# Kernel tuning notes

Hardware: AMD Instinct MI355X
Metric: run time of the kernel (lower is better)

The kernel has to match this reference:

```python
import jax, jax.numpy as jnp
import numpy as np

N, C, H, W = 4, 64, 64, 64
EPS = 1e-5


def setup_inputs() -> dict:
    key = jax.random.key(0)
    ks = jax.random.split(key, 8)
    f = lambda k, s: jax.random.normal(k, s, dtype=jnp.float32)
    return {
        "low_feats": f(ks[0], (N, C, H, W)),
        "heat0": f(ks[1], (N, C, H, W)),
        "heat1": f(ks[2], (N, C, H, W)),
        # f_query: 1x1 conv + BN(gamma,beta) + ReLU
        "Wq": f(ks[3], (C, C)) * 0.05, "bq": jnp.zeros((C,), jnp.float32),
        "gq": jnp.ones((C,), jnp.float32), "betaq": jnp.zeros((C,), jnp.float32),
        # f_key: 1x1 conv + BN + ReLU
        "Wk": f(ks[4], (C, C)) * 0.05, "bk": jnp.zeros((C,), jnp.float32),
        "gk": jnp.ones((C,), jnp.float32), "betak": jnp.zeros((C,), jnp.float32),
        # f_value: plain 1x1 conv
        "Wv": f(ks[5], (C, C)) * 0.05, "bv": jnp.zeros((C,), jnp.float32),
    }


def _conv1x1(x, Wc, bc):
    # [N,C,H,W] -> [N,O,H,W]
    return jnp.einsum("oc,nchw->nohw", Wc, x) + bc[None, :, None, None]


def _conv_bn_relu(x, Wc, bc, g, beta):
    y = _conv1x1(x, Wc, bc)
    mu = y.mean(axis=(0, 2, 3), keepdims=True)      # batch-stat BN (train mode)
    var = y.var(axis=(0, 2, 3), keepdims=True)
    y = (y - mu) * jax.lax.rsqrt(var + EPS)
    y = y * g[None, :, None, None] + beta[None, :, None, None]
    return jax.nn.relu(y)


def reference(low_feats, heat0, heat1, Wq, bq, gq, betaq, Wk, bk, gk, betak, Wv, bv):
    n, c, h, w = low_feats.shape
    hw = h * w
    query = _conv_bn_relu(low_feats, Wq, bq, gq, betaq).reshape(n, c, hw).transpose(0, 2, 1)  # [N,HW,C]
    keym = _conv_bn_relu(low_feats, Wk, bk, gk, betak).reshape(n, c, hw)                      # [N,C,HW]
    value = _conv1x1(low_feats, Wv, bv).reshape(n, c, hw).transpose(0, 2, 1)                  # [N,HW,C]
    sim = jax.nn.softmax(jnp.einsum("nqc,nck->nqk", query, keym), axis=-1)                    # [N,HW,HW]
    # dual gated value paths share the softmax map: sim@vI + sim@vC == sim@(vI+vC)
    gate = (heat0 + heat1).reshape(n, c, hw).transpose(0, 2, 1)                               # [N,HW,C]
    gated_v = gate * value
    ctx = jnp.einsum("nqk,nkc->nqc", sim, gated_v)                                            # [N,HW,C]
    return ctx.transpose(0, 2, 1).reshape(n, c, h, w)
```

## Files before the change

### kernel.cpp

```cpp
#include <hip/hip_runtime.h>

#define NB 4
#define CC 64
#define HW 4096
#define NT (NB*HW)
#define EPSV 1e-5f
#define LOG2E 1.4426950408889634f

typedef _Float16 f16;
typedef _Float16 half4 __attribute__((ext_vector_type(4)));
typedef _Float16 half8 __attribute__((ext_vector_type(8)));
typedef float   float4v __attribute__((ext_vector_type(4)));

#define NELEM ((size_t)NB*HW*CC)
#define NSLOT 128

#define PART_OFF 512
#define TEN_OFF  264192

__global__ __launch_bounds__(256)
void conv2_kernel(const float* __restrict__ x,
                  const float* __restrict__ h0, const float* __restrict__ h1,
                  const float* __restrict__ Wq, const float* __restrict__ bq,
                  const float* __restrict__ Wk, const float* __restrict__ bk,
                  const float* __restrict__ Wv, const float* __restrict__ bv,
                  float* __restrict__ ws,
                  f16* __restrict__ q, f16* __restrict__ k, f16* __restrict__ gv)
{
    __shared__ float Wl[3][16*CC];
    __shared__ float xs[CC][128];
    const int t    = threadIdx.x;
    const int n    = blockIdx.y;
    const int z    = blockIdx.z;
    const int px0  = blockIdx.x * 128;
    const int lane = t & 63;
    const int grp  = t >> 6;
    const int ocl  = grp * 4;
    const int oc0  = z*16 + ocl;

    ((float4*)Wl[0])[t] = ((const float4*)(Wq + (size_t)z*16*CC))[t];
    ((float4*)Wl[1])[t] = ((const float4*)(Wk + (size_t)z*16*CC))[t];
    ((float4*)Wl[2])[t] = ((const float4*)(Wv + (size_t)z*16*CC))[t];
    for (int i = t; i < CC*32; i += 256) {
        int ic = i >> 5, c4 = i & 31;
        ((float4*)&xs[ic][0])[c4] =
            ((const float4*)(x + ((size_t)n*CC + ic)*HW + px0))[c4];
    }
    __syncthreads();

    float aq[4][2], ak[4][2], av[4][2];
    #pragma unroll
    for (int j = 0; j < 4; ++j) {
        aq[j][0] = aq[j][1] = bq[oc0+j];
        ak[j][0] = ak[j][1] = bk[oc0+j];
        av[j][0] = av[j][1] = bv[oc0+j];
    }

    for (int ic = 0; ic < CC; ic += 4) {
        float2 xv0 = *(float2*)&xs[ic  ][lane*2];
        float2 xv1 = *(float2*)&xs[ic+1][lane*2];
        float2 xv2 = *(float2*)&xs[ic+2][lane*2];
        float2 xv3 = *(float2*)&xs[ic+3][lane*2];
        #pragma unroll
        for (int j = 0; j < 4; ++j) {
            const int row = (ocl+j)*CC + ic;
            float4 wq = *(const float4*)&Wl[0][row];
            float4 wk = *(const float4*)&Wl[1][row];
            float4 wv = *(const float4*)&Wl[2][row];
            aq[j][0] = fmaf(wq.x,xv0.x, fmaf(wq.y,xv1.x, fmaf(wq.z,xv2.x, fmaf(wq.w,xv3.x, aq[j][0]))));
            aq[j][1] = fmaf(wq.x,xv0.y, fmaf(wq.y,xv1.y, fmaf(wq.z,xv2.y, fmaf(wq.w,xv3.y, aq[j][1]))));
            ak[j][0] = fmaf(wk.x,xv0.x, fmaf(wk.y,xv1.x, fmaf(wk.z,xv2.x, fmaf(wk.w,xv3.x, ak[j][0]))));
            ak[j][1] = fmaf(wk.x,xv0.y, fmaf(wk.y,xv1.y, fmaf(wk.z,xv2.y, fmaf(wk.w,xv3.y, ak[j][1]))));
            av[j][0] = fmaf(wv.x,xv0.x, fmaf(wv.y,xv1.x, fmaf(wv.z,xv2.x, fmaf(wv.w,xv3.x, av[j][0]))));
            av[j][1] = fmaf(wv.x,xv0.y, fmaf(wv.y,xv1.y, fmaf(wv.z,xv2.y, fmaf(wv.w,xv3.y, av[j][1]))));
        }
    }

    const int px = px0 + lane*2;
    const size_t base = ((size_t)n*HW + px)*CC + oc0;
    half4 vq0, vq1, vk0, vk1;
    #pragma unroll
    for (int j = 0; j < 4; ++j) {
        vq0[j] = (f16)aq[j][0]; vq1[j] = (f16)aq[j][1];
        vk0[j] = (f16)ak[j][0]; vk1[j] = (f16)ak[j][1];
    }
    *(half4*)&q[base]      = vq0;  *(half4*)&q[base + CC] = vq1;
    *(half4*)&k[base]      = vk0;  *(half4*)&k[base + CC] = vk1;

    #pragma unroll
    for (int j = 0; j < 4; ++j) {
        size_t gi = ((size_t)n*CC + oc0 + j)*HW + px;
        f16 g0 = (f16)((h0[gi]   + h1[gi]  ) * av[j][0]);
        f16 g1 = (f16)((h0[gi+1] + h1[gi+1]) * av[j][1]);
        gv[gi]   = g0;
        gv[gi+1] = g1;
    }

    float* slot = ws + PART_OFF + (size_t)(n*(HW/128) + blockIdx.x)*256;
    #pragma unroll
    for (int j = 0; j < 4; ++j) {
        float v0 = aq[j][0] + aq[j][1];
        float v1 = aq[j][0]*aq[j][0] + aq[j][1]*aq[j][1];
        float v2 = ak[j][0] + ak[j][1];
        float v3 = ak[j][0]*ak[j][0] + ak[j][1]*ak[j][1];
        #pragma unroll
        for (int off = 32; off > 0; off >>= 1) {
            v0 += __shfl_down(v0, off);
            v1 += __shfl_down(v1, off);
            v2 += __shfl_down(v2, off);
            v3 += __shfl_down(v3, off);
        }
        if (lane == 0) {
            slot[      oc0 + j] = v0;
            slot[ 64 + oc0 + j] = v1;
            slot[128 + oc0 + j] = v2;
            slot[192 + oc0 + j] = v3;
        }
    }
}

__global__ __launch_bounds__(256)
void apply_kernel(f16* __restrict__ q, f16* __restrict__ k,
                  const float* __restrict__ ws,
                  const float* __restrict__ gq, const float* __restrict__ betaq,
                  const float* __restrict__ gk, const float* __restrict__ betak)
{
    __shared__ float tot[128];
    __shared__ float sc[CC], sh[CC];
    const int t = threadIdx.x;
    const int tens = blockIdx.y;

    if (t < 128) {
        const float* base = ws + PART_OFF + tens*128 + t;
        float acc = 0.0f;
        #pragma unroll 8
        for (int s = 0; s < NSLOT; ++s) acc += base[(size_t)s*256];
        tot[t] = acc;
    }
    __syncthreads();
    if (t < 64) {
        float mean = tot[t] * (1.0f / NT);
        float var  = tot[64 + t] * (1.0f / NT) - mean*mean;
        if (tens == 0) {
            float s = gq[t] * rsqrtf(var + EPSV);
            sc[t] = s;  sh[t] = betaq[t] - mean*s;
        } else {
            float s = gk[t] * rsqrtf(var + EPSV);
            sc[t] = s * LOG2E;  sh[t] = (betak[t] - mean*s) * LOG2E;
        }
    }
    __syncthreads();

    f16* p = tens ? k : q;
    const size_t e0 = ((size_t)blockIdx.x * 256 + t) * 16;
    const int c0 = (int)(e0 & 63);

    half8 v0 = *(half8*)&p[e0], v1 = *(half8*)&p[e0 + 8];
    half8 o0, o1;
    #pragma unroll
    for (int j = 0; j < 8; ++j) {
        o0[j] = (f16)fmaxf(fmaf(sc[c0+j],   (float)v0[j], sh[c0+j]),   0.0f);
        o1[j] = (f16)fmaxf(fmaf(sc[c0+8+j], (float)v1[j], sh[c0+8+j]), 0.0f);
    }
    *(half8*)&p[e0]     = o0;
    *(half8*)&p[e0 + 8] = o1;
}

__global__ __launch_bounds__(512, 4)
void attn_kernel(const f16* __restrict__ q, const f16* __restrict__ k,
                 const f16* __restrict__ gv, float* __restrict__ out)
{
    __shared__ float Obuf[8][4][256];
    __shared__ float MLbuf[2][8][32];

    const int t    = threadIdx.x;
    const int n    = blockIdx.y;
    const int w    = t >> 6;
    const int lane = t & 63;
    const int m16  = lane & 15;
    const int kb   = lane >> 4;
    const int q0   = blockIdx.x * 32;

    half8 qf[2][2];
    #pragma unroll
    for (int qt = 0; qt < 2; ++qt) {
        const size_t qb = ((size_t)n*HW + q0 + qt*16 + m16)*CC + kb*8;
        qf[qt][0] = *(const half8*)&q[qb];
        qf[qt][1] = *(const half8*)&q[qb + 32];
    }

    const int    kt0   = w * 512;
    const size_t krow  = (size_t)n*HW*CC;
    const size_t gbase = ((size_t)n*CC + m16)*HW;

    half8 khf[2][2];
    half4 gvf[2][4];
    const half4 ones = {(f16)1.f, (f16)1.f, (f16)1.f, (f16)1.f};

#define LOADK(KT) do {                                                        \
    size_t a_ = krow + ((size_t)(KT) + m16)*CC + kb*8;                        \
    khf[0][0] = *(const half8*)&k[a_];                                        \
    khf[0][1] = *(const half8*)&k[a_ + 32];                                   \
    khf[1][0] = *(const half8*)&k[a_ + 16*CC];                                \
    khf[1][1] = *(const half8*)&k[a_ + 16*CC + 32];                           \
} while (0)

#define LOADGV(KT) do {                                                       \
    size_t g_ = gbase + (size_t)(KT) + kb*4;                                  \
    _Pragma("unroll") for (int k2_ = 0; k2_ < 2; ++k2_)                       \
    _Pragma("unroll") for (int ct_ = 0; ct_ < 4; ++ct_)                       \
        gvf[k2_][ct_] = *(const half4*)&gv[g_ + k2_*16 + (size_t)ct_*16*HW];  \
} while (0)

    float4v accO[2][4], accL[2];
    #pragma unroll
    for (int qt = 0; qt < 2; ++qt) {
        #pragma unroll
        for (int ct = 0; ct < 4; ++ct) accO[qt][ct] = (float4v){0.f,0.f,0.f,0.f};
        accL[qt] = (float4v){0.f,0.f,0.f,0.f};
    }
    float m[2] = {-INFINITY,-INFINITY};

#define STEP(KTN) do {                                                        \
    LOADK(KTN);                                                               \
    LOADGV(KTN);                                                              \
    float4v accS[2][2];                                                       \
    _Pragma("unroll") for (int qt_ = 0; qt_ < 2; ++qt_)                       \
    _Pragma("unroll") for (int k2_ = 0; k2_ < 2; ++k2_) {                     \
        float4v z_ = {0.f,0.f,0.f,0.f};                                       \
        z_ = __builtin_amdgcn_mfma_f32_16x16x32_f16(khf[k2_][0], qf[qt_][0], z_, 0,0,0); \
        accS[qt_][k2_] = __builtin_amdgcn_mfma_f32_16x16x32_f16(khf[k2_][1], qf[qt_][1], z_, 0,0,0); \
    }                                                                         \
    float mx[2];                                                              \
    _Pragma("unroll") for (int qt_ = 0; qt_ < 2; ++qt_) {                     \
        float v_ = fmaxf(fmaxf(fmaxf(accS[qt_][0][0], accS[qt_][0][1]),       \
                               fmaxf(accS[qt_][0][2], accS[qt_][0][3])),      \
                         fmaxf(fmaxf(accS[qt_][1][0], accS[qt_][1][1]),       \
                               fmaxf(accS[qt_][1][2], accS[qt_][1][3])));     \
        v_ = fmaxf(v_, __shfl_xor(v_, 16));                                   \
        v_ = fmaxf(v_, __shfl_xor(v_, 32));                                   \
        mx[qt_] = v_;                                                         \
    }                                                                         \
    int need_ = (mx[0] > m[0]) | (mx[1] > m[1]);                              \
    if (__any(need_)) {                                                       \
        _Pragma("unroll") for (int qt_ = 0; qt_ < 2; ++qt_) {                 \
            float mn_ = fmaxf(m[qt_], mx[qt_]);                               \
            float al_ = exp2f(m[qt_] - mn_);                                  \
            m[qt_] = mn_;                                                     \
            accL[qt_][0]*=al_; accL[qt_][1]*=al_;                             \
            accL[qt_][2]*=al_; accL[qt_][3]*=al_;                             \
            _Pragma("unroll") for (int ct_ = 0; ct_ < 4; ++ct_) {             \
                accO[qt_][ct_][0]*=al_; accO[qt_][ct_][1]*=al_;               \
                accO[qt_][ct_][2]*=al_; accO[qt_][ct_][3]*=al_;               \
            }                                                                 \
        }                                                                     \
    }                                                                         \
    _Pragma("unroll") for (int qt_ = 0; qt_ < 2; ++qt_) {                     \
        float p0 = exp2f(accS[qt_][0][0]-m[qt_]), p1 = exp2f(accS[qt_][0][1]-m[qt_]); \
        float p2 = exp2f(accS[qt_][0][2]-m[qt_]), p3 = exp2f(accS[qt_][0][3]-m[qt_]); \
        float p4 = exp2f(accS[qt_][1][0]-m[qt_]), p5 = exp2f(accS[qt_][1][1]-m[qt_]); \
        float p6 = exp2f(accS[qt_][1][2]-m[qt_]), p7 = exp2f(accS[qt_][1][3]-m[qt_]); \
        half4 pfa, pfb;                                                       \
        pfa[0]=(f16)p0; pfa[1]=(f16)p1; pfa[2]=(f16)p2; pfa[3]=(f16)p3;       \
        pfb[0]=(f16)p4; pfb[1]=(f16)p5; pfb[2]=(f16)p6; pfb[3]=(f16)p7;       \
        accL[qt_] = __builtin_amdgcn_mfma_f32_16x16x16f16(ones, pfa, accL[qt_], 0,0,0); \
        accL[qt_] = __builtin_amdgcn_mfma_f32_16x16x16f16(ones, pfb, accL[qt_], 0,0,0); \
        _Pragma("unroll") for (int ct_ = 0; ct_ < 4; ++ct_) {                 \
            float4v o_ = accO[qt_][ct_];                                      \
            o_ = __builtin_amdgcn_mfma_f32_16x16x16f16(gvf[0][ct_], pfa, o_, 0,0,0); \
            accO[qt_][ct_] = __builtin_amdgcn_mfma_f32_16x16x16f16(gvf[1][ct_], pfb, o_, 0,0,0); \
        }                                                                     \
    }                                                                         \
} while (0)

    for (int i2 = 0; i2 < 16; ++i2) {
        STEP(kt0 + i2*32);
    }

    if (kb == 0) {
        #pragma unroll
        for (int qt = 0; qt < 2; ++qt) {
            MLbuf[0][w][qt*16 + m16] = m[qt];
            MLbuf[1][w][qt*16 + m16] = accL[qt][0];
        }
    }
    __syncthreads();

    float invL[2];
    #pragma unroll
    for (int qt = 0; qt < 2; ++qt) {
        const int r = qt*16 + m16;
        float M = MLbuf[0][0][r];
        #pragma unroll
        for (int src = 1; src < 8; ++src) M = fmaxf(M, MLbuf[0][src][r]);
        float L = 0.0f;
        #pragma unroll
        for (int src = 0; src < 8; ++src)
            L += MLbuf[1][src][r] * exp2f(MLbuf[0][src][r] - M);
        const float f = exp2f(m[qt] - M);
        #pragma unroll
        for (int ct = 0; ct < 4; ++ct) {
            accO[qt][ct][0] *= f; accO[qt][ct][1] *= f;
            accO[qt][ct][2] *= f; accO[qt][ct][3] *= f;
        }
        invL[qt] = 1.0f / L;
    }

    for (int rd = 0; rd < 2; ++rd) {
        __syncthreads();
        #pragma unroll
        for (int ct = 0; ct < 4; ++ct)
            ((float4*)&Obuf[w][ct][0])[lane] =
                (float4){accO[rd][ct][0], accO[rd][ct][1], accO[rd][ct][2], accO[rd][ct][3]};
        __syncthreads();
        if (w < 4) {
            float4 s = ((float4*)&Obuf[0][w][0])[lane];
            #pragma unroll
            for (int src = 1; src < 8; ++src) {
                float4 v = ((float4*)&Obuf[src][w][0])[lane];
                s.x += v.x; s.y += v.y; s.z += v.z; s.w += v.w;
            }
            const float iv = invL[rd];
            const int chb = w*16 + kb*4;
            const int row = q0 + rd*16 + m16;
            out[((size_t)n*CC + chb + 0)*HW + row] = s.x * iv;
            out[((size_t)n*CC + chb + 1)*HW + row] = s.y * iv;
            out[((size_t)n*CC + chb + 2)*HW + row] = s.z * iv;
            out[((size_t)n*CC + chb + 3)*HW + row] = s.w * iv;
        }
    }
#undef STEP
#undef LOADGV
#undef LOADK
}

extern "C" void kernel_launch(void* const* d_in, const int* in_sizes, int n_in,
                              void* d_out, int out_size, void* d_ws, size_t ws_size,
                              hipStream_t stream)
{
    const float* low   = (const float*)d_in[0];
    const float* h0    = (const float*)d_in[1];
    const float* h1    = (const float*)d_in[2];
    const float* Wq    = (const float*)d_in[3];
    const float* bq    = (const float*)d_in[4];
    const float* gq    = (const float*)d_in[5];
    const float* betaq = (const float*)d_in[6];
    const float* Wk    = (const float*)d_in[7];
    const float* bk    = (const float*)d_in[8];
    const float* gk    = (const float*)d_in[9];
    const float* betak = (const float*)d_in[10];
    const float* Wv    = (const float*)d_in[11];
    const float* bv    = (const float*)d_in[12];

    float* wsf = (float*)d_ws;
    float* out = (float*)d_out;

    f16* q  = (f16*)((char*)d_ws + TEN_OFF);
    f16* k  = q + NELEM;
    f16* gv = k + NELEM;

    conv2_kernel<<<dim3(HW/128, NB, 4), 256, 0, stream>>>(
        low, h0, h1, Wq, bq, Wk, bk, Wv, bv, wsf, q, k, gv);

    apply_kernel<<<dim3((int)(NELEM/(256*16)), 2), 256, 0, stream>>>(
        q, k, wsf, gq, betaq, gk, betak);

    attn_kernel<<<dim3(HW/32, NB), 512, 0, stream>>>(q, k, gv, out);
}
```

Before: 190.2 us.

## Stage K and gated-V tiles through swizzled LDS with double buffering in attention

Restructures the attention kernel so K and gated-value tiles are loaded cooperatively into double-buffered, XOR-swizzled shared memory and shared by two query-tile warps, instead of each warp reading them from global memory. Warps are re-split as 2 query tiles × 4 key slices, so each warp handles one 16-row query tile over 1024 keys. It also adds a lazy max-rescale threshold so rescaling happens only when the running max grows by more than 8, and replaces the MFMA row-sum with scalar adds. The costs are more barriers per iteration and 64KB of LDS per block, which may limit occupancy.

After: 160.2 us. 1.19x faster.

```diff
diff --git a/kernel.cpp b/kernel.cpp
--- a/kernel.cpp
+++ b/kernel.cpp
@@ -6,6 +6,7 @@
 #define NT (NB*HW)
 #define EPSV 1e-5f
 #define LOG2E 1.4426950408889634f
+#define THRV 8.0f
 
 typedef _Float16 f16;
 typedef _Float16 half4 __attribute__((ext_vector_type(4)));
@@ -170,8 +171,11 @@
 void attn_kernel(const f16* __restrict__ q, const f16* __restrict__ k,
                  const f16* __restrict__ gv, float* __restrict__ out)
 {
-    __shared__ float Obuf[8][4][256];
-    __shared__ float MLbuf[2][8][32];
+    __shared__ alignas(16) char SM[65536];
+    f16 (* const Ks)[2][2048]    = reinterpret_cast<f16(*)[2][2048]>(SM);
+    f16 (* const GVs)[2][2048]   = reinterpret_cast<f16(*)[2][2048]>(SM + 32768);
+    float (* const Obuf)[4][256] = reinterpret_cast<float(*)[4][256]>(SM);
+    float (* const MLbuf)[8][16] = reinterpret_cast<float(*)[8][16]>(SM + 32768);
 
     const int t    = threadIdx.x;
     const int n    = blockIdx.y;
@@ -179,159 +183,184 @@
     const int lane = t & 63;
     const int m16  = lane & 15;
     const int kb   = lane >> 4;
-    const int q0   = blockIdx.x * 32;
-
-    half8 qf[2][2];
-    #pragma unroll
-    for (int qt = 0; qt < 2; ++qt) {
-        const size_t qb = ((size_t)n*HW + q0 + qt*16 + m16)*CC + kb*8;
-        qf[qt][0] = *(const half8*)&q[qb];
-        qf[qt][1] = *(const half8*)&q[qb + 32];
-    }
-
-    const int    kt0   = w * 512;
-    const size_t krow  = (size_t)n*HW*CC;
-    const size_t gbase = ((size_t)n*CC + m16)*HW;
-
-    half8 khf[2][2];
-    half4 gvf[2][4];
-    const half4 ones = {(f16)1.f, (f16)1.f, (f16)1.f, (f16)1.f};
-
-#define LOADK(KT) do {                                                        \
-    size_t a_ = krow + ((size_t)(KT) + m16)*CC + kb*8;                        \
-    khf[0][0] = *(const half8*)&k[a_];                                        \
-    khf[0][1] = *(const half8*)&k[a_ + 32];                                   \
-    khf[1][0] = *(const half8*)&k[a_ + 16*CC];                                \
-    khf[1][1] = *(const half8*)&k[a_ + 16*CC + 32];                           \
+    const int qi   = w >> 2;
+    const int si   = w & 3;
+    const int q0g  = blockIdx.x * 32 + qi * 16;
+
+    half8 qf0, qf1;
+    {
+        const size_t qb = ((size_t)n*HW + q0g + m16)*CC + kb*8;
+        qf0 = *(const half8*)&q[qb];
+        qf1 = *(const half8*)&q[qb + 32];
+    }
+
+    const f16* kn  = k  + (size_t)n*HW*CC;
+    const f16* gvn = gv + (size_t)n*CC*HW;
+
+    const int rl  = lane >> 3, cl  = lane & 7;
+    const int chl = lane >> 2, kcl = lane & 3;
+    const int    srcK = rl*CC + cl*8;
+    const int    dstK = rl*CC + ((cl ^ rl) * 8);
+    const size_t srcG = (size_t)chl*HW + kcl*8;
+    const int    dstG = chl*32 + ((kcl ^ (chl & 3)) * 8);
+
+    const int kt00 = si * 1024;
+
+    const int swzk = (m16 & 7) << 3;
+    const int swzg = (m16 & 3) << 3;
+    const int e0k  = (kb*8)      ^ swzk;
+    const int e1k  = (kb*8 + 32) ^ swzk;
+
+    half8 stg[4];
+
+#define STAGE_LOAD(IT) do {                                                   \
+    const int kt_ = kt00 + (IT)*32;                                           \
+    if (qi == 0) {                                                            \
+        const f16* s_ = kn + (size_t)kt_*CC + srcK;                           \
+        stg[0] = *(const half8*)(s_);                                         \
+        stg[1] = *(const half8*)(s_ +  8*CC);                                 \
+        stg[2] = *(const half8*)(s_ + 16*CC);                                 \
+        stg[3] = *(const half8*)(s_ + 24*CC);                                 \
+    } else {                                                                  \
+        const f16* s_ = gvn + srcG + kt_;                                     \
+        stg[0] = *(const half8*)(s_);                                         \
+        stg[1] = *(const half8*)(s_ + (size_t)16*HW);                         \
+        stg[2] = *(const half8*)(s_ + (size_t)32*HW);                         \
+        stg[3] = *(const half8*)(s_ + (size_t)48*HW);                         \
+    }                                                                         \
 } while (0)
 
-#define LOADGV(KT) do {                                                       \
-    size_t g_ = gbase + (size_t)(KT) + kb*4;                                  \
-    _Pragma("unroll") for (int k2_ = 0; k2_ < 2; ++k2_)                       \
-    _Pragma("unroll") for (int ct_ = 0; ct_ < 4; ++ct_)                       \
-        gvf[k2_][ct_] = *(const half4*)&gv[g_ + k2_*16 + (size_t)ct_*16*HW];  \
+#define STAGE_WRITE(BUF) do {                                                 \
+    if (qi == 0) {                                                            \
+        f16* d_ = &Ks[si][BUF][dstK];                                         \
+        *(half8*)(d_)        = stg[0];                                        \
+        *(half8*)(d_ +  512) = stg[1];                                        \
+        *(half8*)(d_ + 1024) = stg[2];                                        \
+        *(half8*)(d_ + 1536) = stg[3];                                        \
+    } else {                                                                  \
+        f16* d_ = &GVs[si][BUF][dstG];                                        \
+        *(half8*)(d_)        = stg[0];                                        \
+        *(half8*)(d_ +  512) = stg[1];                                        \
+        *(half8*)(d_ + 1024) = stg[2];                                        \
+        *(half8*)(d_ + 1536) = stg[3];                                        \
+    }                                                                         \
 } while (0)
 
-    float4v accO[2][4], accL[2];
-    #pragma unroll
-    for (int qt = 0; qt < 2; ++qt) {
-        #pragma unroll
-        for (int ct = 0; ct < 4; ++ct) accO[qt][ct] = (float4v){0.f,0.f,0.f,0.f};
-        accL[qt] = (float4v){0.f,0.f,0.f,0.f};
-    }
-    float m[2] = {-INFINITY,-INFINITY};
-
-#define STEP(KTN) do {                                                        \
-    LOADK(KTN);                                                               \
-    LOADGV(KTN);                                                              \
-    float4v accS[2][2];                                                       \
-    _Pragma("unroll") for (int qt_ = 0; qt_ < 2; ++qt_)                       \
-    _Pragma("unroll") for (int k2_ = 0; k2_ < 2; ++k2_) {                     \
-        float4v z_ = {0.f,0.f,0.f,0.f};                                       \
-        z_ = __builtin_amdgcn_mfma_f32_16x16x32_f16(khf[k2_][0], qf[qt_][0], z_, 0,0,0); \
-        accS[qt_][k2_] = __builtin_amdgcn_mfma_f32_16x16x32_f16(khf[k2_][1], qf[qt_][1], z_, 0,0,0); \
-    }                                                                         \
-    float mx[2];                                                              \
-    _Pragma("unroll") for (int qt_ = 0; qt_ < 2; ++qt_) {                     \
-        float v_ = fmaxf(fmaxf(fmaxf(accS[qt_][0][0], accS[qt_][0][1]),       \
-                               fmaxf(accS[qt_][0][2], accS[qt_][0][3])),      \
-                         fmaxf(fmaxf(accS[qt_][1][0], accS[qt_][1][1]),       \
-                               fmaxf(accS[qt_][1][2], accS[qt_][1][3])));     \
-        v_ = fmaxf(v_, __shfl_xor(v_, 16));                                   \
-        v_ = fmaxf(v_, __shfl_xor(v_, 32));                                   \
-        mx[qt_] = v_;                                                         \
-    }                                                                         \
-    int need_ = (mx[0] > m[0]) | (mx[1] > m[1]);                              \
-    if (__any(need_)) {                                                       \
-        _Pragma("unroll") for (int qt_ = 0; qt_ < 2; ++qt_) {                 \
-            float mn_ = fmaxf(m[qt_], mx[qt_]);                               \
-            float al_ = exp2f(m[qt_] - mn_);                                  \
-            m[qt_] = mn_;                                                     \
-            accL[qt_][0]*=al_; accL[qt_][1]*=al_;                             \
-            accL[qt_][2]*=al_; accL[qt_][3]*=al_;                             \
-            _Pragma("unroll") for (int ct_ = 0; ct_ < 4; ++ct_) {             \
-                accO[qt_][ct_][0]*=al_; accO[qt_][ct_][1]*=al_;               \
-                accO[qt_][ct_][2]*=al_; accO[qt_][ct_][3]*=al_;               \
-            }                                                                 \
+    float4v accO[4];
+    #pragma unroll
+    for (int ct = 0; ct < 4; ++ct) accO[ct] = (float4v){0.f,0.f,0.f,0.f};
+    float accL = 0.0f;
+    float mreg = -INFINITY;
+
+#define COMPUTE(CUR) do {                                                     \
+    const f16* Kb_ = &Ks[si][CUR][0];                                         \
+    const f16* Gb_ = &GVs[si][CUR][0];                                        \
+    half8 kh00_ = *(const half8*)&Kb_[ m16*CC       + e0k];                   \
+    half8 kh01_ = *(const half8*)&Kb_[ m16*CC       + e1k];                   \
+    half8 kh10_ = *(const half8*)&Kb_[(m16+16)*CC   + e0k];                   \
+    half8 kh11_ = *(const half8*)&Kb_[(m16+16)*CC   + e1k];                   \
+    float4v s0_ = {0.f,0.f,0.f,0.f}, s1_ = {0.f,0.f,0.f,0.f};                 \
+    s0_ = __builtin_amdgcn_mfma_f32_16x16x32_f16(kh00_, qf0, s0_, 0,0,0);     \
+    s0_ = __builtin_amdgcn_mfma_f32_16x16x32_f16(kh01_, qf1, s0_, 0,0,0);     \
+    s1_ = __builtin_amdgcn_mfma_f32_16x16x32_f16(kh10_, qf0, s1_, 0,0,0);     \
+    s1_ = __builtin_amdgcn_mfma_f32_16x16x32_f16(kh11_, qf1, s1_, 0,0,0);     \
+    float v_ = fmaxf(fmaxf(fmaxf(s0_[0],s0_[1]), fmaxf(s0_[2],s0_[3])),       \
+                     fmaxf(fmaxf(s1_[0],s1_[1]), fmaxf(s1_[2],s1_[3])));      \
+    v_ = fmaxf(v_, __shfl_xor(v_, 16));                                       \
+    v_ = fmaxf(v_, __shfl_xor(v_, 32));                                       \
+    if (__any(v_ > mreg + THRV)) {                                            \
+        float mn_ = fmaxf(mreg, v_);                                          \
+        float al_ = exp2f(mreg - mn_);                                        \
+        mreg = mn_;  accL *= al_;                                             \
+        _Pragma("unroll") for (int ct_ = 0; ct_ < 4; ++ct_) {                 \
+            accO[ct_][0]*=al_; accO[ct_][1]*=al_;                             \
+            accO[ct_][2]*=al_; accO[ct_][3]*=al_;                             \
         }                                                                     \
     }                                                                         \
-    _Pragma("unroll") for (int qt_ = 0; qt_ < 2; ++qt_) {                     \
-        float p0 = exp2f(accS[qt_][0][0]-m[qt_]), p1 = exp2f(accS[qt_][0][1]-m[qt_]); \
-        float p2 = exp2f(accS[qt_][0][2]-m[qt_]), p3 = exp2f(accS[qt_][0][3]-m[qt_]); \
-        float p4 = exp2f(accS[qt_][1][0]-m[qt_]), p5 = exp2f(accS[qt_][1][1]-m[qt_]); \
-        float p6 = exp2f(accS[qt_][1][2]-m[qt_]), p7 = exp2f(accS[qt_][1][3]-m[qt_]); \
-        half4 pfa, pfb;                                                       \
-        pfa[0]=(f16)p0; pfa[1]=(f16)p1; pfa[2]=(f16)p2; pfa[3]=(f16)p3;       \
-        pfb[0]=(f16)p4; pfb[1]=(f16)p5; pfb[2]=(f16)p6; pfb[3]=(f16)p7;       \
-        accL[qt_] = __builtin_amdgcn_mfma_f32_16x16x16f16(ones, pfa, accL[qt_], 0,0,0); \
-        accL[qt_] = __builtin_amdgcn_mfma_f32_16x16x16f16(ones, pfb, accL[qt_], 0,0,0); \
-        _Pragma("unroll") for (int ct_ = 0; ct_ < 4; ++ct_) {                 \
-            float4v o_ = accO[qt_][ct_];                                      \
-            o_ = __builtin_amdgcn_mfma_f32_16x16x16f16(gvf[0][ct_], pfa, o_, 0,0,0); \
-            accO[qt_][ct_] = __builtin_amdgcn_mfma_f32_16x16x16f16(gvf[1][ct_], pfb, o_, 0,0,0); \
-        }                                                                     \
+    float p0_=exp2f(s0_[0]-mreg), p1_=exp2f(s0_[1]-mreg);                     \
+    float p2_=exp2f(s0_[2]-mreg), p3_=exp2f(s0_[3]-mreg);                     \
+    float p4_=exp2f(s1_[0]-mreg), p5_=exp2f(s1_[1]-mreg);                     \
+    float p6_=exp2f(s1_[2]-mreg), p7_=exp2f(s1_[3]-mreg);                     \
+    accL += ((p0_+p1_)+(p2_+p3_)) + ((p4_+p5_)+(p6_+p7_));                    \
+    half4 pfa_, pfb_;                                                         \
+    pfa_[0]=(f16)p0_; pfa_[1]=(f16)p1_; pfa_[2]=(f16)p2_; pfa_[3]=(f16)p3_;   \
+    pfb_[0]=(f16)p4_; pfb_[1]=(f16)p5_; pfb_[2]=(f16)p6_; pfb_[3]=(f16)p7_;   \
+    _Pragma("unroll") for (int ct_ = 0; ct_ < 4; ++ct_) {                     \
+        const int gb_ = (ct_*16 + m16)*32;                                    \
+        half4 g0_ = *(const half4*)&Gb_[gb_ + ((kb*4)      ^ swzg)];          \
+        half4 g1_ = *(const half4*)&Gb_[gb_ + ((kb*4 + 16) ^ swzg)];          \
+        float4v o_ = accO[ct_];                                               \
+        o_ = __builtin_amdgcn_mfma_f32_16x16x16f16(g0_, pfa_, o_, 0,0,0);     \
+        accO[ct_] = __builtin_amdgcn_mfma_f32_16x16x16f16(g1_, pfb_, o_, 0,0,0); \
     }                                                                         \
 } while (0)
 
-    for (int i2 = 0; i2 < 16; ++i2) {
-        STEP(kt0 + i2*32);
-    }
-
+    STAGE_LOAD(0);
+    STAGE_WRITE(0);
+    __syncthreads();
+
+    for (int it = 0; it < 31; ++it) {
+        const int cur = it & 1;
+        STAGE_LOAD(it + 1);
+        COMPUTE(cur);
+        STAGE_WRITE(cur ^ 1);
+        __syncthreads();
+    }
+    COMPUTE(1);
+
+    float lq = accL;
+    lq += __shfl_xor(lq, 16);
+    lq += __shfl_xor(lq, 32);
     if (kb == 0) {
-        #pragma unroll
-        for (int qt = 0; qt < 2; ++qt) {
-            MLbuf[0][w][qt*16 + m16] = m[qt];
-            MLbuf[1][w][qt*16 + m16] = accL[qt][0];
-        }
-    }
-    __syncthreads();
-
-    float invL[2];
-    #pragma unroll
-    for (int qt = 0; qt < 2; ++qt) {
-        const int r = qt*16 + m16;
-        float M = MLbuf[0][0][r];
-        #pragma unroll
-        for (int src = 1; src < 8; ++src) M = fmaxf(M, MLbuf[0][src][r]);
-        float L = 0.0f;
-        #pragma unroll
-        for (int src = 0; src < 8; ++src)
-            L += MLbuf[1][src][r] * exp2f(MLbuf[0][src][r] - M);
-        const float f = exp2f(m[qt] - M);
+        MLbuf[0][w][m16] = mreg;
+        MLbuf[1][w][m16] = lq;
+    }
+    __syncthreads();
+
+    const int wb = qi * 4;
+    {
+        float M_ = fmaxf(fmaxf(MLbuf[0][wb][m16],   MLbuf[0][wb+1][m16]),
+                         fmaxf(MLbuf[0][wb+2][m16], MLbuf[0][wb+3][m16]));
+        float f_ = exp2f(mreg - M_);
         #pragma unroll
         for (int ct = 0; ct < 4; ++ct) {
-            accO[qt][ct][0] *= f; accO[qt][ct][1] *= f;
-            accO[qt][ct][2] *= f; accO[qt][ct][3] *= f;
-        }
-        invL[qt] = 1.0f / L;
-    }
-
-    for (int rd = 0; rd < 2; ++rd) {
-        __syncthreads();
-        #pragma unroll
-        for (int ct = 0; ct < 4; ++ct)
-            ((float4*)&Obuf[w][ct][0])[lane] =
-                (float4){accO[rd][ct][0], accO[rd][ct][1], accO[rd][ct][2], accO[rd][ct][3]};
-        __syncthreads();
-        if (w < 4) {
-            float4 s = ((float4*)&Obuf[0][w][0])[lane];
-            #pragma unroll
-            for (int src = 1; src < 8; ++src) {
-                float4 v = ((float4*)&Obuf[src][w][0])[lane];
-                s.x += v.x; s.y += v.y; s.z += v.z; s.w += v.w;
-            }
-            const float iv = invL[rd];
-            const int chb = w*16 + kb*4;
-            const int row = q0 + rd*16 + m16;
-            out[((size_t)n*CC + chb + 0)*HW + row] = s.x * iv;
-            out[((size_t)n*CC + chb + 1)*HW + row] = s.y * iv;
-            out[((size_t)n*CC + chb + 2)*HW + row] = s.z * iv;
-            out[((size_t)n*CC + chb + 3)*HW + row] = s.w * iv;
-        }
-    }
-#undef STEP
-#undef LOADGV
-#undef LOADK
+            accO[ct][0]*=f_; accO[ct][1]*=f_; accO[ct][2]*=f_; accO[ct][3]*=f_;
+        }
+    }
+    #pragma unroll
+    for (int ct = 0; ct < 4; ++ct)
+        ((float4*)&Obuf[w][ct][0])[lane] =
+            (float4){accO[ct][0], accO[ct][1], accO[ct][2], accO[ct][3]};
+    __syncthreads();
+
+    {
+        const int qi2 = w >> 2, ct2 = w & 3, wb2 = qi2 * 4;
+        float4 s  = ((float4*)&Obuf[wb2  ][ct2][0])[lane];
+        float4 a1 = ((float4*)&Obuf[wb2+1][ct2][0])[lane];
+        float4 a2 = ((float4*)&Obuf[wb2+2][ct2][0])[lane];
+        float4 a3 = ((float4*)&Obuf[wb2+3][ct2][0])[lane];
+        s.x += a1.x + a2.x + a3.x;
+        s.y += a1.y + a2.y + a3.y;
+        s.z += a1.z + a2.z + a3.z;
+        s.w += a1.w + a2.w + a3.w;
+        float m0 = MLbuf[0][wb2  ][m16], m1 = MLbuf[0][wb2+1][m16];
+        float m2 = MLbuf[0][wb2+2][m16], m3 = MLbuf[0][wb2+3][m16];
+        float M_ = fmaxf(fmaxf(m0, m1), fmaxf(m2, m3));
+        float L_ = MLbuf[1][wb2  ][m16] * exp2f(m0 - M_)
+                 + MLbuf[1][wb2+1][m16] * exp2f(m1 - M_)
+                 + MLbuf[1][wb2+2][m16] * exp2f(m2 - M_)
+                 + MLbuf[1][wb2+3][m16] * exp2f(m3 - M_);
+        const float iv = 1.0f / L_;
+        const int chb = ct2*16 + kb*4;
+        const int row = blockIdx.x*32 + qi2*16 + m16;
+        out[((size_t)n*CC + chb + 0)*HW + row] = s.x * iv;
+        out[((size_t)n*CC + chb + 1)*HW + row] = s.y * iv;
+        out[((size_t)n*CC + chb + 2)*HW + row] = s.z * iv;
+        out[((size_t)n*CC + chb + 3)*HW + row] = s.w * iv;
+    }
+#undef COMPUTE
+#undef STAGE_WRITE
+#undef STAGE_LOAD
 }
 
 extern "C" void kernel_launch(void* const* d_in, const int* in_sizes, int n_in,
```
